# Performance work log

Measured on AMD Instinct MI355X. Metric: run time of the kernel, lower is better.

## Reference

```python
import jax, jax.numpy as jnp
import numpy as np

N_NODES = 50000
N_EDGES = 800000
IN_DIM = 128
HIDDEN = 128


def setup_inputs() -> dict:
    key = jax.random.key(0)
    ks = jax.random.split(key, 6)
    x = jax.random.normal(ks[0], (N_NODES, IN_DIM), dtype=jnp.float32)
    edge_index = jax.random.randint(ks[1], (2, N_EDGES), 0, N_NODES, dtype=jnp.int32)
    W1 = jax.random.normal(ks[2], (IN_DIM, HIDDEN), dtype=jnp.float32) * 0.05
    b1 = jnp.zeros((HIDDEN,), dtype=jnp.float32)
    W2 = jax.random.normal(ks[3], (HIDDEN, HIDDEN), dtype=jnp.float32) * 0.05
    b2 = jnp.zeros((HIDDEN,), dtype=jnp.float32)
    return {"x": x, "edge_index": edge_index, "W1": W1, "b1": b1, "W2": W2, "b2": b2}


def _gcn_conv(x, W, b, src, dst, norm, n):
    # PyG GCNConv: linear transform, then normalized sum-aggregate, then bias.
    h = x @ W                                  # [N, H]
    msg = h[src] * norm[:, None]               # gather + scale  [E+N, H]
    out = jax.ops.segment_sum(msg, dst, num_segments=n)
    return out + b


def reference(x, edge_index, W1, b1, W2, b2):
    n = x.shape[0]
    # add self-loops (GCNConv default add_self_loops=True)
    loops = jnp.arange(n, dtype=edge_index.dtype)
    src = jnp.concatenate([edge_index[0], loops])
    dst = jnp.concatenate([edge_index[1], loops])
    # symmetric normalization: deg over destination nodes (edge_weight = 1)
    deg = jax.ops.segment_sum(jnp.ones(src.shape, dtype=x.dtype), dst, num_segments=n)
    dinv = jax.lax.rsqrt(deg)                  # deg >= 1 because of self-loops
    norm = dinv[src] * dinv[dst]               # [E+N]
    h = jax.nn.relu(_gcn_conv(x, W1, b1, src, dst, norm, n))
    return _gcn_conv(h, W2, b2, src, dst, norm, n)
```

## Files before the change

### kernel.cpp

```cpp
#include <hip/hip_runtime.h>

#define N_NODES 50000
#define N_EDGES 800000
#define DIM 128
#define CHUNK 4096
#define GRID 196
#define SEG_CAP 6144
#define GEMM_BLOCKS 391
#define GA 196
#define GB (GEMM_BLOCKS - GA)

typedef __attribute__((ext_vector_type(8))) short bf16x8;
typedef __attribute__((ext_vector_type(4))) float f32x4;


__device__ inline unsigned rne_bf16(float f) {
    unsigned u = __float_as_uint(f);
    return (u + 0x7FFFu + ((u >> 16) & 1u)) >> 16;
}
__device__ inline unsigned pk_bf16(float a, float b) {
    return rne_bf16(a) | (rne_bf16(b) << 16);
}
__device__ inline float bf_lo(unsigned u) { return __uint_as_float(u << 16); }
__device__ inline float bf_hi(unsigned u) { return __uint_as_float(u & 0xFFFF0000u); }


__device__ void fragw_build(const float* __restrict__ W, uint4* __restrict__ fh,
                            uint4* __restrict__ fl, int slot) {
    const int lane = slot & 63, tile = slot >> 6;
    const int c = tile >> 2, q = tile & 3;
    const int k0 = q * 32 + ((lane >> 4) << 3);
    const int col = c * 16 + (lane & 15);
    unsigned h[8], l[8];
#pragma unroll
    for (int j = 0; j < 8; ++j) {
        float w = W[(size_t)(k0 + j) * DIM + col];
        unsigned hb = rne_bf16(w);
        h[j] = hb;
        l[j] = rne_bf16(w - __uint_as_float(hb << 16));
    }
    uint4 uh, ul;
    uh.x = h[0] | (h[1] << 16); uh.y = h[2] | (h[3] << 16);
    uh.z = h[4] | (h[5] << 16); uh.w = h[6] | (h[7] << 16);
    ul.x = l[0] | (l[1] << 16); ul.y = l[2] | (l[3] << 16);
    ul.z = l[4] | (l[5] << 16); ul.w = l[6] | (l[7] << 16);
    fh[slot] = uh;
    fl[slot] = ul;
}


__global__ __launch_bounds__(256) void chunk_hist_fragw(const int* __restrict__ dst,
                                                        int* __restrict__ chist,
                                                        const float* __restrict__ W1,
                                                        const float* __restrict__ W2,
                                                        uint4* f1h, uint4* f1l,
                                                        uint4* f2h, uint4* f2l) {
    const int bid = blockIdx.x;
    if (bid < GRID) {
        __shared__ int hist[256];
        const int t = threadIdx.x;
        const int eb = bid * CHUNK;
        const int cnt = min(CHUNK, N_EDGES - eb);
        hist[t] = 0;
        __syncthreads();
        for (int i = t; i < cnt; i += 256)
            atomicAdd(&hist[dst[eb + i] >> 8], 1);
        __syncthreads();
        chist[bid * 256 + t] = hist[t];
    } else {
        const int b2 = bid - GRID;
        const int slot = (b2 & 7) * 256 + threadIdx.x;
        if (b2 < 8) fragw_build(W1, f1h, f1l, slot);
        else        fragw_build(W2, f2h, f2l, slot);
    }
}


__device__ void gemm_body(const float* __restrict__ X,
                          const uint4* __restrict__ fWh,
                          const uint4* __restrict__ fWl,
                          uint2* __restrict__ O, int gb, char* smem) {
    const int t = threadIdx.x;

    {
        uint4* s4 = (uint4*)smem;
        for (int i = t; i < 2048; i += 256) {
            s4[i] = fWh[i];
            s4[2048 + i] = fWl[i];
        }
    }
    __syncthreads();

    const int w = t >> 6, lane = t & 63;
    const int lrow = lane & 15, lgrp = lane >> 4;
    const int rbase = gb * 128;

    bf16x8 Ah[2][4], Al[2][4];
#pragma unroll
    for (int m = 0; m < 2; ++m) {
        const int r = rbase + w * 32 + m * 16 + lrow;
        const bool ok = (r < N_NODES);
        const float4* xp = (const float4*)(X + (size_t)r * DIM + lgrp * 8);
#pragma unroll
        for (int q = 0; q < 4; ++q) {
            float4 a0 = ok ? xp[q * 8]     : make_float4(0.f, 0.f, 0.f, 0.f);
            float4 a1 = ok ? xp[q * 8 + 1] : make_float4(0.f, 0.f, 0.f, 0.f);
            float f[8] = {a0.x, a0.y, a0.z, a0.w, a1.x, a1.y, a1.z, a1.w};
            bf16x8 hi, lo;
#pragma unroll
            for (int j = 0; j < 8; ++j) {
                unsigned hb = rne_bf16(f[j]);
                hi[j] = (short)hb;
                lo[j] = (short)rne_bf16(f[j] - __uint_as_float(hb << 16));
            }
            Ah[m][q] = hi;
            Al[m][q] = lo;
        }
    }

    f32x4 acc[2][8];
#pragma unroll
    for (int m = 0; m < 2; ++m)
#pragma unroll
        for (int c = 0; c < 8; ++c)
            acc[m][c] = (f32x4){0.f, 0.f, 0.f, 0.f};

    const bf16x8* Bh = (const bf16x8*)smem;
    const bf16x8* Bl = (const bf16x8*)(smem + 32768);
#pragma unroll
    for (int c = 0; c < 8; ++c) {
#pragma unroll
        for (int q = 0; q < 4; ++q) {
            bf16x8 bh = Bh[(c * 4 + q) * 64 + lane];
            bf16x8 bl = Bl[(c * 4 + q) * 64 + lane];
#pragma unroll
            for (int m = 0; m < 2; ++m) {
                acc[m][c] = __builtin_amdgcn_mfma_f32_16x16x32_bf16(Ah[m][q], bh, acc[m][c], 0, 0, 0);
                acc[m][c] = __builtin_amdgcn_mfma_f32_16x16x32_bf16(Al[m][q], bh, acc[m][c], 0, 0, 0);
                acc[m][c] = __builtin_amdgcn_mfma_f32_16x16x32_bf16(Ah[m][q], bl, acc[m][c], 0, 0, 0);
            }
        }
    }

    __syncthreads();
    float* Lf = (float*)smem;
#pragma unroll
    for (int m = 0; m < 2; ++m)
#pragma unroll
        for (int c = 0; c < 8; ++c)
#pragma unroll
            for (int rg = 0; rg < 4; ++rg)
                Lf[(w * 32 + m * 16 + lgrp * 4 + rg) * DIM + c * 16 + lrow] = acc[m][c][rg];
    __syncthreads();

    const float4* Lf4 = (const float4*)smem;
    for (int idx = t; idx < 4096; idx += 256) {
        const int row = idx >> 5, s = idx & 31;
        const int gr = rbase + row;
        if (gr < N_NODES) {
            float4 v = Lf4[idx];
            uint2 o;
            o.x = pk_bf16(v.x, v.y);
            o.y = pk_bf16(v.z, v.w);
            O[(size_t)gr * 32 + s] = o;
        }
    }
}


__device__ void sort_scatter_body(const int* __restrict__ src,
                                  const int* __restrict__ dst,
                                  const int* __restrict__ chist,
                                  unsigned* __restrict__ sorted,
                                  int bid, char* smem) {
    int* hist  = (int*)smem;
    int* sc    = hist + 256;
    int* lbase = sc + 256;
    int* lcur  = lbase + 256;
    int* gbase = lcur + 256;
    unsigned* sl = (unsigned*)(smem + 5 * 1024);

    const int t = threadIdx.x;
    const int eb = bid * CHUNK;
    const int cnt = min(CHUNK, N_EDGES - eb);

    int sum = 0, myoff = 0;
    for (int c = 0; c < GRID; ++c) {
        int v = chist[c * 256 + t];
        if (c == bid) myoff = sum;
        sum += v;
    }
    hist[t] = chist[bid * 256 + t];
    sc[t] = sum;
    __syncthreads();
    for (int off = 1; off < 256; off <<= 1) {
        int u = (t >= off) ? sc[t - off] : 0;
        __syncthreads();
        sc[t] += u;
        __syncthreads();
    }
    gbase[t] = (sc[t] - sum) + myoff;
    __syncthreads();

    sc[t] = hist[t];
    __syncthreads();
    for (int off = 1; off < 256; off <<= 1) {
        int u = (t >= off) ? sc[t - off] : 0;
        __syncthreads();
        sc[t] += u;
        __syncthreads();
    }
    int ex = sc[t] - hist[t];
    lbase[t] = ex;
    lcur[t] = ex;
    __syncthreads();

    for (int i = t; i < cnt; i += 256) {
        int s = src[eb + i], d = dst[eb + i];
        int b = d >> 8;
        int p = atomicAdd(&lcur[b], 1);
        sl[p] = ((unsigned)b << 24) | ((unsigned)(d & 255) << 16) | (unsigned)s;
    }
    __syncthreads();
    for (int i = t; i < cnt; i += 256) {
        unsigned rec = sl[i];
        int b = rec >> 24;
        sorted[gbase[b] + (i - lbase[b])] = rec;
    }
}


__device__ void csr_build_body(const unsigned* __restrict__ sorted,
                               const int* __restrict__ chist,
                               int* __restrict__ rowptr,
                               float* __restrict__ dinv,
                               int* __restrict__ csr,
                               int k, char* smem) {
    int* hist    = (int*)smem;
    int* sc      = hist + 256;
    int* lcur    = sc + 256;
    int* bbase_s = lcur + 256;
    int* cnt_s   = bbase_s + 256;
    int* seg     = (int*)(smem + 5 * 1024);

    const int t = threadIdx.x;

    int sum = 0;
    for (int c = 0; c < GRID; ++c) sum += chist[c * 256 + t];
    cnt_s[t] = sum;
    sc[t] = sum;
    __syncthreads();
    for (int off = 1; off < 256; off <<= 1) {
        int u = (t >= off) ? sc[t - off] : 0;
        __syncthreads();
        sc[t] += u;
        __syncthreads();
    }
    bbase_s[t] = sc[t] - cnt_s[t];
    __syncthreads();
    const int base = bbase_s[k];
    const int cntk = cnt_s[k];
    if (k == 0 && t == 0) rowptr[N_NODES] = N_EDGES;

    hist[t] = 0;
    __syncthreads();
    for (int i = t; i < cntk; i += 256)
        atomicAdd(&hist[(sorted[base + i] >> 16) & 255], 1);
    __syncthreads();

    const int node = (k << 8) + t;
    const int dv = hist[t];
    if (node < N_NODES) dinv[node] = rsqrtf((float)dv + 1.0f);

    sc[t] = dv;
    __syncthreads();
    for (int off = 1; off < 256; off <<= 1) {
        int u = (t >= off) ? sc[t - off] : 0;
        __syncthreads();
        sc[t] += u;
        __syncthreads();
    }
    int ex = sc[t] - dv;
    if (node < N_NODES) rowptr[node] = base + ex;
    lcur[t] = ex;
    __syncthreads();

    if (cntk <= SEG_CAP) {
        for (int i = t; i < cntk; i += 256) {
            unsigned rec = sorted[base + i];
            int p = atomicAdd(&lcur[(rec >> 16) & 255], 1);
            seg[p] = (int)(rec & 0xFFFFu);
        }
        __syncthreads();
        for (int i = t; i < cntk; i += 256)
            csr[base + i] = seg[i];
    } else {
        for (int i = t; i < cntk; i += 256) {
            unsigned rec = sorted[base + i];
            int p = atomicAdd(&lcur[(rec >> 16) & 255], 1);
            csr[base + p] = (int)(rec & 0xFFFFu);
        }
    }
}


__global__ __launch_bounds__(256, 2) void sort_gemm(const int* __restrict__ src,
                                                    const int* __restrict__ dst,
                                                    const int* __restrict__ chist,
                                                    unsigned* __restrict__ sorted,
                                                    const float* __restrict__ X,
                                                    const uint4* __restrict__ fWh,
                                                    const uint4* __restrict__ fWl,
                                                    uint2* __restrict__ O) {
    __shared__ __align__(16) char smem[65536];
    if (blockIdx.x < GRID)
        sort_scatter_body(src, dst, chist, sorted, blockIdx.x, smem);
    else
        gemm_body(X, fWh, fWl, O, blockIdx.x - GRID, smem);
}

__global__ __launch_bounds__(256, 2) void csr_gemm(const unsigned* __restrict__ sorted,
                                                   const int* __restrict__ chist,
                                                   int* __restrict__ rowptr,
                                                   float* __restrict__ dinv,
                                                   int* __restrict__ csr,
                                                   const float* __restrict__ X,
                                                   const uint4* __restrict__ fWh,
                                                   const uint4* __restrict__ fWl,
                                                   uint2* __restrict__ O) {
    __shared__ __align__(16) char smem[65536];
    if (blockIdx.x < GRID)
        csr_build_body(sorted, chist, rowptr, dinv, csr, blockIdx.x, smem);
    else
        gemm_body(X, fWh, fWl, O, blockIdx.x - GRID + GA, smem);
}

__global__ __launch_bounds__(256, 2) void gemm_xw(const float* __restrict__ X,
                                                  const uint4* __restrict__ fWh,
                                                  const uint4* __restrict__ fWl,
                                                  uint2* __restrict__ O) {
    __shared__ __align__(16) char smem[65536];
    gemm_body(X, fWh, fWl, O, blockIdx.x, smem);
}


__global__ __launch_bounds__(256) void aggregate_kernel(const uint2* __restrict__ H2,
                                                        const int* __restrict__ rowptr,
                                                        const int* __restrict__ csr,
                                                        const float* __restrict__ dinv,
                                                        const float4* __restrict__ b4,
                                                        float4* __restrict__ out,
                                                        int relu) {
    int node = blockIdx.x * 4 + (threadIdx.x >> 6);
    if (node >= N_NODES) return;
    const int lane = threadIdx.x & 63;
    const int half = lane >> 5;
    const int col  = lane & 31;

    const float dn = dinv[node];
    float4 acc = make_float4(0.f, 0.f, 0.f, 0.f);
    if (half == 0) {
        uint2 v = H2[(size_t)node * 32 + col];
        acc.x = dn * bf_lo(v.x); acc.y = dn * bf_hi(v.x);
        acc.z = dn * bf_lo(v.y); acc.w = dn * bf_hi(v.y);
    }

    int j = rowptr[node];
    const int end = rowptr[node + 1];

#define ACC(v, ds) do { \
        acc.x = fmaf((ds), bf_lo((v).x), acc.x); \
        acc.y = fmaf((ds), bf_hi((v).x), acc.y); \
        acc.z = fmaf((ds), bf_lo((v).y), acc.z); \
        acc.w = fmaf((ds), bf_hi((v).y), acc.w); } while (0)

    for (; j + 16 <= end; j += 16) {
        int s0 = csr[j +  0 + half], s1 = csr[j +  2 + half];
        int s2 = csr[j +  4 + half], s3 = csr[j +  6 + half];
        int s4 = csr[j +  8 + half], s5 = csr[j + 10 + half];
        int s6 = csr[j + 12 + half], s7 = csr[j + 14 + half];
        uint2 v0 = H2[(size_t)s0 * 32 + col]; float d0 = dinv[s0];
        uint2 v1 = H2[(size_t)s1 * 32 + col]; float d1 = dinv[s1];
        uint2 v2 = H2[(size_t)s2 * 32 + col]; float d2 = dinv[s2];
        uint2 v3 = H2[(size_t)s3 * 32 + col]; float d3 = dinv[s3];
        uint2 v4 = H2[(size_t)s4 * 32 + col]; float d4 = dinv[s4];
        uint2 v5 = H2[(size_t)s5 * 32 + col]; float d5 = dinv[s5];
        uint2 v6 = H2[(size_t)s6 * 32 + col]; float d6 = dinv[s6];
        uint2 v7 = H2[(size_t)s7 * 32 + col]; float d7 = dinv[s7];
        ACC(v0, d0); ACC(v1, d1); ACC(v2, d2); ACC(v3, d3);
        ACC(v4, d4); ACC(v5, d5); ACC(v6, d6); ACC(v7, d7);
    }
    if (j + 8 <= end) {
        int s0 = csr[j + half], s1 = csr[j + 2 + half];
        int s2 = csr[j + 4 + half], s3 = csr[j + 6 + half];
        uint2 v0 = H2[(size_t)s0 * 32 + col]; float d0 = dinv[s0];
        uint2 v1 = H2[(size_t)s1 * 32 + col]; float d1 = dinv[s1];
        uint2 v2 = H2[(size_t)s2 * 32 + col]; float d2 = dinv[s2];
        uint2 v3 = H2[(size_t)s3 * 32 + col]; float d3 = dinv[s3];
        ACC(v0, d0); ACC(v1, d1); ACC(v2, d2); ACC(v3, d3);
        j += 8;
    }
    if (j + 4 <= end) {
        int s0 = csr[j + half], s1 = csr[j + 2 + half];
        uint2 v0 = H2[(size_t)s0 * 32 + col]; float d0 = dinv[s0];
        uint2 v1 = H2[(size_t)s1 * 32 + col]; float d1 = dinv[s1];
        ACC(v0, d0); ACC(v1, d1);
        j += 4;
    }
    if (j + 2 <= end) {
        int s = csr[j + half];
        uint2 v = H2[(size_t)s * 32 + col]; float d0 = dinv[s];
        ACC(v, d0);
        j += 2;
    }
    if (j < end && half == 0) {
        int s = csr[j];
        uint2 v = H2[(size_t)s * 32 + col]; float d0 = dinv[s];
        ACC(v, d0);
    }
#undef ACC

    acc.x += __shfl_xor(acc.x, 32, 64);
    acc.y += __shfl_xor(acc.y, 32, 64);
    acc.z += __shfl_xor(acc.z, 32, 64);
    acc.w += __shfl_xor(acc.w, 32, 64);

    if (half == 0) {
        float4 bb = b4[col];
        float4 o;
        o.x = acc.x * dn + bb.x;
        o.y = acc.y * dn + bb.y;
        o.z = acc.z * dn + bb.z;
        o.w = acc.w * dn + bb.w;
        if (relu) {
            o.x = fmaxf(o.x, 0.f); o.y = fmaxf(o.y, 0.f);
            o.z = fmaxf(o.z, 0.f); o.w = fmaxf(o.w, 0.f);
        }
        out[(size_t)node * 32 + col] = o;
    }
}


extern "C" void kernel_launch(void* const* d_in, const int* in_sizes, int n_in,
                              void* d_out, int out_size, void* d_ws, size_t ws_size,
                              hipStream_t stream) {
    const float* x  = (const float*)d_in[0];
    const int*   ei = (const int*)d_in[1];
    const float* W1 = (const float*)d_in[2];
    const float* b1 = (const float*)d_in[3];
    const float* W2 = (const float*)d_in[4];
    const float* b2 = (const float*)d_in[5];
    float* out = (float*)d_out;

    const int* src = ei;
    const int* dst = ei + N_EDGES;

    char* p = (char*)d_ws;
    int*      chist  = (int*)p;              p += GRID * 256 * 4;
    float*    dinv   = (float*)p;            p += ((N_NODES * 4 + 1023) & ~1023);
    int*      rowptr = (int*)p;              p += (((N_NODES + 1) * 4 + 1023) & ~1023);
    unsigned* sorted = (unsigned*)p;         p += ((N_EDGES * 4 + 1023) & ~1023);
    int*      csr    = (int*)p;              p += ((N_EDGES * 4 + 1023) & ~1023);
    uint4*    f1h    = (uint4*)p;            p += 32768;
    uint4*    f1l    = (uint4*)p;            p += 32768;
    uint4*    f2h    = (uint4*)p;            p += 32768;
    uint4*    f2l    = (uint4*)p;            p += 32768;
    uint2*    hp     = (uint2*)p;            p += (size_t)N_NODES * DIM * 2;
    float*    bufB   = (float*)p;

    const int aggBlocks = (N_NODES + 3) / 4;

    chunk_hist_fragw<<<GRID + 16, 256, 0, stream>>>(dst, chist, W1, W2,
                                                    f1h, f1l, f2h, f2l);
    sort_gemm<<<GRID + GA, 256, 0, stream>>>(src, dst, chist, sorted, x, f1h, f1l, hp);
    csr_gemm<<<GRID + GB, 256, 0, stream>>>(sorted, chist, rowptr, dinv, csr,
                                            x, f1h, f1l, hp);

    aggregate_kernel<<<aggBlocks, 256, 0, stream>>>(hp, rowptr, csr, dinv,
                                                    (const float4*)b1, (float4*)bufB, 1);

    gemm_xw<<<GEMM_BLOCKS, 256, 0, stream>>>(bufB, f2h, f2l, hp);
    aggregate_kernel<<<aggBlocks, 256, 0, stream>>>(hp, rowptr, csr, dinv,
                                                    (const float4*)b2, (float4*)out, 0);
}
```

Measured before the change: 217.6 us.

## Fuse layer-1 aggregation with layer-2 GEMM and precompute bucket bases

Layer-1 aggregation is merged into the second GEMM kernel. Each 512-thread block aggregates 128 nodes straight into shared memory as split hi/lo bf16 and then runs the MFMA GEMM, so the fp32 intermediate buffer no longer makes a round trip through global memory and one launch is removed. The CSR build now reads bucket base offsets written by block 0 of the sort kernel instead of every block re-summing the chunk histograms and re-running a scan. The price is lower aggregation parallelism per block, since 8 waves each handle 16 nodes one after another, plus a larger block size.

```diff
diff --git a/kernel.cpp b/kernel.cpp
--- a/kernel.cpp
+++ b/kernel.cpp
@@ -172,6 +172,7 @@
                                   const int* __restrict__ dst,
                                   const int* __restrict__ chist,
                                   unsigned* __restrict__ sorted,
+                                  int* __restrict__ bbase_g,
                                   int bid, char* smem) {
     int* hist  = (int*)smem;
     int* sc    = hist + 256;
@@ -200,6 +201,7 @@
         __syncthreads();
     }
     gbase[t] = (sc[t] - sum) + myoff;
+    if (bid == 0) bbase_g[t] = sc[t] - sum;
     __syncthreads();
 
     sc[t] = hist[t];
@@ -231,35 +233,19 @@
 
 
 __device__ void csr_build_body(const unsigned* __restrict__ sorted,
-                               const int* __restrict__ chist,
+                               const int* __restrict__ bbase,
                                int* __restrict__ rowptr,
                                float* __restrict__ dinv,
                                int* __restrict__ csr,
                                int k, char* smem) {
-    int* hist    = (int*)smem;
-    int* sc      = hist + 256;
-    int* lcur    = sc + 256;
-    int* bbase_s = lcur + 256;
-    int* cnt_s   = bbase_s + 256;
-    int* seg     = (int*)(smem + 5 * 1024);
+    int* hist = (int*)smem;
+    int* sc   = hist + 256;
+    int* lcur = sc + 256;
+    int* seg  = (int*)(smem + 3 * 1024);
 
     const int t = threadIdx.x;
-
-    int sum = 0;
-    for (int c = 0; c < GRID; ++c) sum += chist[c * 256 + t];
-    cnt_s[t] = sum;
-    sc[t] = sum;
-    __syncthreads();
-    for (int off = 1; off < 256; off <<= 1) {
-        int u = (t >= off) ? sc[t - off] : 0;
-        __syncthreads();
-        sc[t] += u;
-        __syncthreads();
-    }
-    bbase_s[t] = sc[t] - cnt_s[t];
-    __syncthreads();
-    const int base = bbase_s[k];
-    const int cntk = cnt_s[k];
+    const int base = bbase[k];
+    const int cntk = ((k == 255) ? N_EDGES : bbase[k + 1]) - base;
     if (k == 0 && t == 0) rowptr[N_NODES] = N_EDGES;
 
     hist[t] = 0;
@@ -308,19 +294,20 @@
                                                     const int* __restrict__ dst,
                                                     const int* __restrict__ chist,
                                                     unsigned* __restrict__ sorted,
+                                                    int* __restrict__ bbase_g,
                                                     const float* __restrict__ X,
                                                     const uint4* __restrict__ fWh,
                                                     const uint4* __restrict__ fWl,
                                                     uint2* __restrict__ O) {
     __shared__ __align__(16) char smem[65536];
     if (blockIdx.x < GRID)
-        sort_scatter_body(src, dst, chist, sorted, blockIdx.x, smem);
+        sort_scatter_body(src, dst, chist, sorted, bbase_g, blockIdx.x, smem);
     else
         gemm_body(X, fWh, fWl, O, blockIdx.x - GRID, smem);
 }
 
 __global__ __launch_bounds__(256, 2) void csr_gemm(const unsigned* __restrict__ sorted,
-                                                   const int* __restrict__ chist,
+                                                   const int* __restrict__ bbase,
                                                    int* __restrict__ rowptr,
                                                    float* __restrict__ dinv,
                                                    int* __restrict__ csr,
@@ -330,29 +317,17 @@
                                                    uint2* __restrict__ O) {
     __shared__ __align__(16) char smem[65536];
     if (blockIdx.x < GRID)
-        csr_build_body(sorted, chist, rowptr, dinv, csr, blockIdx.x, smem);
+        csr_build_body(sorted, bbase, rowptr, dinv, csr, blockIdx.x, smem);
     else
         gemm_body(X, fWh, fWl, O, blockIdx.x - GRID + GA, smem);
 }
 
-__global__ __launch_bounds__(256, 2) void gemm_xw(const float* __restrict__ X,
-                                                  const uint4* __restrict__ fWh,
-                                                  const uint4* __restrict__ fWl,
-                                                  uint2* __restrict__ O) {
-    __shared__ __align__(16) char smem[65536];
-    gemm_body(X, fWh, fWl, O, blockIdx.x, smem);
-}
-
-
-__global__ __launch_bounds__(256) void aggregate_kernel(const uint2* __restrict__ H2,
-                                                        const int* __restrict__ rowptr,
-                                                        const int* __restrict__ csr,
-                                                        const float* __restrict__ dinv,
-                                                        const float4* __restrict__ b4,
-                                                        float4* __restrict__ out,
-                                                        int relu) {
-    int node = blockIdx.x * 4 + (threadIdx.x >> 6);
-    if (node >= N_NODES) return;
+
+__device__ inline float4 agg_node(int node, const uint2* __restrict__ H2,
+                                  const int* __restrict__ rowptr,
+                                  const int* __restrict__ csr,
+                                  const float* __restrict__ dinv,
+                                  const float4* __restrict__ b4, int relu) {
     const int lane = threadIdx.x & 63;
     const int half = lane >> 5;
     const int col  = lane & 31;
@@ -425,9 +400,9 @@
     acc.z += __shfl_xor(acc.z, 32, 64);
     acc.w += __shfl_xor(acc.w, 32, 64);
 
+    float4 o = make_float4(0.f, 0.f, 0.f, 0.f);
     if (half == 0) {
         float4 bb = b4[col];
-        float4 o;
         o.x = acc.x * dn + bb.x;
         o.y = acc.y * dn + bb.y;
         o.z = acc.z * dn + bb.z;
@@ -436,7 +411,107 @@
             o.x = fmaxf(o.x, 0.f); o.y = fmaxf(o.y, 0.f);
             o.z = fmaxf(o.z, 0.f); o.w = fmaxf(o.w, 0.f);
         }
-        out[(size_t)node * 32 + col] = o;
+    }
+    return o;
+}
+
+
+__global__ __launch_bounds__(256) void aggregate_kernel(const uint2* __restrict__ H2,
+                                                        const int* __restrict__ rowptr,
+                                                        const int* __restrict__ csr,
+                                                        const float* __restrict__ dinv,
+                                                        const float4* __restrict__ b4,
+                                                        float4* __restrict__ out,
+                                                        int relu) {
+    int node = blockIdx.x * 4 + (threadIdx.x >> 6);
+    if (node >= N_NODES) return;
+    float4 o = agg_node(node, H2, rowptr, csr, dinv, b4, relu);
+    const int lane = threadIdx.x & 63;
+    if (lane < 32) out[(size_t)node * 32 + lane] = o;
+}
+
+
+__global__ __launch_bounds__(512, 2) void agg_gemm2(const uint2* __restrict__ H2,
+                                                    const int* __restrict__ rowptr,
+                                                    const int* __restrict__ csr,
+                                                    const float* __restrict__ dinv,
+                                                    const float4* __restrict__ b4,
+                                                    const uint4* __restrict__ fWh,
+                                                    const uint4* __restrict__ fWl,
+                                                    uint2* __restrict__ O) {
+    __shared__ __align__(16) char smem[65536];
+    uint2* Hh = (uint2*)smem;
+    uint2* Hl = (uint2*)(smem + 32768);
+    const int t = threadIdx.x;
+    const int w = t >> 6;
+    const int lane = t & 63;
+    const int half = lane >> 5;
+    const int g = lane & 31;
+    const int rbase = blockIdx.x * 128;
+
+    for (int i = 0; i < 16; ++i) {
+        const int row = w * 16 + i;
+        const int node = rbase + row;
+        float4 o = make_float4(0.f, 0.f, 0.f, 0.f);
+        if (node < N_NODES)
+            o = agg_node(node, H2, rowptr, csr, dinv, b4, 1);
+        if (half == 0) {
+            unsigned hx = rne_bf16(o.x), hy = rne_bf16(o.y);
+            unsigned hz = rne_bf16(o.z), hw = rne_bf16(o.w);
+            unsigned lx = rne_bf16(o.x - __uint_as_float(hx << 16));
+            unsigned ly = rne_bf16(o.y - __uint_as_float(hy << 16));
+            unsigned lz = rne_bf16(o.z - __uint_as_float(hz << 16));
+            unsigned lw = rne_bf16(o.w - __uint_as_float(hw << 16));
+            const int idx = row * 32 + (((g >> 1) ^ (row & 7)) << 1) + (g & 1);
+            uint2 hv; hv.x = hx | (hy << 16); hv.y = hz | (hw << 16);
+            uint2 lv; lv.x = lx | (ly << 16); lv.y = lz | (lw << 16);
+            Hh[idx] = hv;
+            Hl[idx] = lv;
+        }
+    }
+    __syncthreads();
+
+    const int lrow = lane & 15, lgrp = lane >> 4;
+    const int arow = w * 16 + lrow;
+    f32x4 acc[8];
+#pragma unroll
+    for (int c = 0; c < 8; ++c) acc[c] = (f32x4){0.f, 0.f, 0.f, 0.f};
+
+#pragma unroll
+    for (int q = 0; q < 4; ++q) {
+        const int idx = arow * 32 + ((((q << 2) + lgrp) ^ (arow & 7)) << 1);
+        bf16x8 Ah = *(const bf16x8*)&Hh[idx];
+        bf16x8 Al = *(const bf16x8*)&Hl[idx];
+#pragma unroll
+        for (int c = 0; c < 8; ++c) {
+            bf16x8 bh = *(const bf16x8*)&fWh[(c * 4 + q) * 64 + lane];
+            bf16x8 bl = *(const bf16x8*)&fWl[(c * 4 + q) * 64 + lane];
+            acc[c] = __builtin_amdgcn_mfma_f32_16x16x32_bf16(Ah, bh, acc[c], 0, 0, 0);
+            acc[c] = __builtin_amdgcn_mfma_f32_16x16x32_bf16(Al, bh, acc[c], 0, 0, 0);
+            acc[c] = __builtin_amdgcn_mfma_f32_16x16x32_bf16(Ah, bl, acc[c], 0, 0, 0);
+        }
+    }
+    __syncthreads();
+
+    float* Lf = (float*)smem;
+#pragma unroll
+    for (int c = 0; c < 8; ++c)
+#pragma unroll
+        for (int rg = 0; rg < 4; ++rg)
+            Lf[(w * 16 + lgrp * 4 + rg) * DIM + c * 16 + lrow] = acc[c][rg];
+    __syncthreads();
+
+    const float4* Lf4 = (const float4*)smem;
+    for (int idx = t; idx < 4096; idx += 512) {
+        const int row = idx >> 5, s = idx & 31;
+        const int gr = rbase + row;
+        if (gr < N_NODES) {
+            float4 v = Lf4[idx];
+            uint2 o2;
+            o2.x = pk_bf16(v.x, v.y);
+            o2.y = pk_bf16(v.z, v.w);
+            O[(size_t)gr * 32 + s] = o2;
+        }
     }
 }
 
@@ -461,25 +536,26 @@
     int*      rowptr = (int*)p;              p += (((N_NODES + 1) * 4 + 1023) & ~1023);
     unsigned* sorted = (unsigned*)p;         p += ((N_EDGES * 4 + 1023) & ~1023);
     int*      csr    = (int*)p;              p += ((N_EDGES * 4 + 1023) & ~1023);
+    int*      bbase  = (int*)p;              p += 1024;
     uint4*    f1h    = (uint4*)p;            p += 32768;
     uint4*    f1l    = (uint4*)p;            p += 32768;
     uint4*    f2h    = (uint4*)p;            p += 32768;
     uint4*    f2l    = (uint4*)p;            p += 32768;
     uint2*    hp     = (uint2*)p;            p += (size_t)N_NODES * DIM * 2;
-    float*    bufB   = (float*)p;
+    uint2*    hp2    = (uint2*)p;
 
     const int aggBlocks = (N_NODES + 3) / 4;
 
     chunk_hist_fragw<<<GRID + 16, 256, 0, stream>>>(dst, chist, W1, W2,
                                                     f1h, f1l, f2h, f2l);
-    sort_gemm<<<GRID + GA, 256, 0, stream>>>(src, dst, chist, sorted, x, f1h, f1l, hp);
-    csr_gemm<<<GRID + GB, 256, 0, stream>>>(sorted, chist, rowptr, dinv, csr,
+    sort_gemm<<<GRID + GA, 256, 0, stream>>>(src, dst, chist, sorted, bbase,
+                                             x, f1h, f1l, hp);
+    csr_gemm<<<GRID + GB, 256, 0, stream>>>(sorted, bbase, rowptr, dinv, csr,
                                             x, f1h, f1l, hp);
 
-    aggregate_kernel<<<aggBlocks, 256, 0, stream>>>(hp, rowptr, csr, dinv,
-                                                    (const float4*)b1, (float4*)bufB, 1);
-
-    gemm_xw<<<GEMM_BLOCKS, 256, 0, stream>>>(bufB, f2h, f2l, hp);
-    aggregate_kernel<<<aggBlocks, 256, 0, stream>>>(hp, rowptr, csr, dinv,
+    agg_gemm2<<<GEMM_BLOCKS, 512, 0, stream>>>(hp, rowptr, csr, dinv,
+                                               (const float4*)b1, f2h, f2l, hp2);
+
+    aggregate_kernel<<<aggBlocks, 256, 0, stream>>>(hp2, rowptr, csr, dinv,
                                                     (const float4*)b2, (float4*)out, 0);
 }
```

After: 228.5 us. 5.0% more time.
